# Performance work log

Measured on AMD Instinct MI355X. Metric: run time of the kernel, lower is better.

Reference implementation:

```python
import jax, jax.numpy as jnp
import numpy as np

TIME_STEP = 0.02  # matches init_kwargs
B, T, D = 128, 2048, 4


def setup_inputs() -> dict:
    key = jax.random.key(0)
    k1, k2, k3, k4 = jax.random.split(key, 4)
    return {
        "h_real": jax.random.normal(k1, (B, T, D, D), dtype=jnp.float32),
        "h_imag": jax.random.normal(k2, (B, T, D, D), dtype=jnp.float32),
        "s_real": jax.random.normal(k3, (B, D, D), dtype=jnp.float32),
        "s_imag": jax.random.normal(k4, (B, D, D), dtype=jnp.float32),
    }


def reference(h_real, h_imag, s_real, s_imag):
    # dt = -1j * time_step (complex64 scalar, as in the keras cell)
    dt = jnp.asarray(-1j * TIME_STEP, dtype=jnp.complex64)
    H = (h_real + 1j * h_imag).astype(jnp.complex64)        # [B,T,D,D]
    state0 = (s_real + 1j * s_imag).astype(jnp.complex64)    # [B,D,D]
    Hs = jnp.transpose(H, (1, 0, 2, 3))                       # [T,B,D,D] for scan

    def step(state, h_t):
        # unitary = expm(-i*dt*H_t), batched over B via expm's leading-dim batching
        unitary = jax.scipy.linalg.expm(h_t * dt)             # [B,D,D]
        new_state = jnp.matmul(unitary, state)                # [B,D,D]
        return new_state, new_state

    _, seq = jax.lax.scan(step, state0, Hs)                   # seq: [T,B,D,D] complex64
    # return real/imag stacked so downstream harness sees a real tensor
    return jnp.stack([seq.real, seq.imag])                    # [2,T,B,D,D] float32
```

## Files before the change

kernel.cpp:

```cpp
#include <hip/hip_runtime.h>

namespace {

constexpr int    TT    = 2048;
constexpr int    BB    = 128;
constexpr int    CHUNK = 8;
constexpr int    TPB   = 1024;
constexpr int    TLOC  = TPB / 2;
constexpr int    BPB   = TT / TLOC;
constexpr int    NBLK  = (BB / 2) * BPB;
constexpr int    NCH   = TLOC / CHUNK;
constexpr float  DT    = 0.02f;
constexpr size_t HALF  = (size_t)TT * BB * 16;

typedef float f32x4 __attribute__((ext_vector_type(4)));

__device__ __forceinline__ void cmm(const float* __restrict__ ar, const float* __restrict__ ai,
                                    const float* __restrict__ br, const float* __restrict__ bi,
                                    float* __restrict__ cr, float* __restrict__ ci) {
#pragma unroll
    for (int i = 0; i < 4; ++i) {
#pragma unroll
        for (int j = 0; j < 4; ++j) {
            float sr = 0.f, si = 0.f;
#pragma unroll
            for (int k = 0; k < 4; ++k) {
                const float xr = ar[i * 4 + k], xi = ai[i * 4 + k];
                const float yr = br[k * 4 + j], yi = bi[k * 4 + j];
                sr = fmaf(xr, yr, sr);
                sr = fmaf(-xi, yi, sr);
                si = fmaf(xr, yi, si);
                si = fmaf(xi, yr, si);
            }
            cr[i * 4 + j] = sr;
            ci[i * 4 + j] = si;
        }
    }
}

__device__ __forceinline__ void cmm_acc(const float* __restrict__ ar, const float* __restrict__ ai,
                                        const float* __restrict__ br, const float* __restrict__ bi,
                                        float* __restrict__ cr, float* __restrict__ ci) {
#pragma unroll
    for (int i = 0; i < 4; ++i) {
#pragma unroll
        for (int j = 0; j < 4; ++j) {
            float sr = cr[i * 4 + j], si = ci[i * 4 + j];
#pragma unroll
            for (int k = 0; k < 4; ++k) {
                const float xr = ar[i * 4 + k], xi = ai[i * 4 + k];
                const float yr = br[k * 4 + j], yi = bi[k * 4 + j];
                sr = fmaf(xr, yr, sr);
                sr = fmaf(-xi, yi, sr);
                si = fmaf(xr, yi, si);
                si = fmaf(xi, yr, si);
            }
            cr[i * 4 + j] = sr;
            ci[i * 4 + j] = si;
        }
    }
}

__device__ __forceinline__ void loadA(const float* __restrict__ hr, const float* __restrict__ hi,
                                      size_t gi, float* __restrict__ a_r, float* __restrict__ a_i) {
    const f32x4* p4r = reinterpret_cast<const f32x4*>(hr) + gi * 4;
    const f32x4* p4i = reinterpret_cast<const f32x4*>(hi) + gi * 4;
#pragma unroll
    for (int v = 0; v < 4; ++v) {
        const f32x4 rr = __builtin_nontemporal_load(p4r + v);
        const f32x4 im = __builtin_nontemporal_load(p4i + v);
#pragma unroll
        for (int e = 0; e < 4; ++e) {
            a_r[v * 4 + e] = DT * im[e];
            a_i[v * 4 + e] = -DT * rr[e];
        }
    }
}

__device__ __forceinline__ void expmPS(const float* __restrict__ a_r, const float* __restrict__ a_i,
                                       float* __restrict__ er, float* __restrict__ ei) {
    float a2r[16], a2i[16];
    cmm(a_r, a_i, a_r, a_i, a2r, a2i);
    float t6r[16], t6i[16];
#pragma unroll
    for (int e = 0; e < 16; ++e) {
        const float d = (e % 5 == 0) ? 1.0f : 0.0f;
        t6r[e] = fmaf(a_r[e], 1.f / 6.f, d * 0.5f);
        t6r[e] = fmaf(a2r[e], 1.f / 24.f, t6r[e]);
        t6i[e] = a_i[e] * (1.f / 6.f);
        t6i[e] = fmaf(a2i[e], 1.f / 24.f, t6i[e]);
        er[e]  = a_r[e] + d;
        ei[e]  = a_i[e];
    }
    cmm_acc(a2r, a2i, t6r, t6i, er, ei);
}

__device__ __forceinline__ unsigned int cp_load(unsigned int* p) {
    return __hip_atomic_fetch_add(p, 0u, __ATOMIC_RELAXED, __HIP_MEMORY_SCOPE_AGENT);
}
__device__ __forceinline__ void cp_store(unsigned int* p, unsigned int v) {
    (void)__hip_atomic_exchange(p, v, __ATOMIC_RELAXED, __HIP_MEMORY_SCOPE_AGENT);
}

}

__global__ void k_init(unsigned int* flag) { flag[threadIdx.x] = 0u; }

__global__ __launch_bounds__(TPB, 4) void k_main(
        const float* __restrict__ hr, const float* __restrict__ hi,
        const float* __restrict__ sr, const float* __restrict__ si,
        float* __restrict__ out, float* __restrict__ prefix,
        unsigned int* __restrict__ flag) {
    __shared__ float lds[24576];
    float* tot  = lds;
    float* carr = lds + 4096;

    const int tid    = threadIdx.x;
    const int bid    = blockIdx.x;
    const int blockT = bid & (BPB - 1);
    const int pair   = bid >> 2;
    const int b0     = pair * 2;
    const int pb     = tid & 1;
    const int tloc   = tid >> 1;
    const int t      = blockT * TLOC + tloc;
    const int b      = b0 + pb;
    const int lane   = tid & 63;
    const int sub    = (lane >> 1) & (CHUNK - 1);
    const int c      = tloc >> 3;

    float er[16], ei[16];
    {
        float a_r[16], a_i[16];
        loadA(hr, hi, (size_t)b * TT + t, a_r, a_i);
        expmPS(a_r, a_i, er, ei);
    }

#pragma unroll
    for (int d = 1; d < CHUNK; d <<= 1) {
        int src = lane - 2 * d;
        if (src < 0) src = 0;
        float qr[16], qi[16];
#pragma unroll
        for (int e = 0; e < 16; ++e) {
            qr[e] = __shfl(er[e], src, 64);
            qi[e] = __shfl(ei[e], src, 64);
        }
        float nr[16], ni[16];
        cmm(er, ei, qr, qi, nr, ni);
        const bool pred = (sub >= d);
#pragma unroll
        for (int e = 0; e < 16; ++e) {
            er[e] = pred ? nr[e] : er[e];
            ei[e] = pred ? ni[e] : ei[e];
        }
    }

    if (sub == CHUNK - 1) {
#pragma unroll
        for (int e = 0; e < 16; ++e) {
            tot[((pb << 5) + e) * NCH + c]      = er[e];
            tot[((pb << 5) + 16 + e) * NCH + c] = ei[e];
        }
    }
    __syncthreads();

    if (tid < 128) {
        const int w  = tid >> 6;
        const int cc = tid & 63;
        float ipr[16], ipi[16];
#pragma unroll
        for (int e = 0; e < 16; ++e) {
            ipr[e] = tot[((w << 5) + e) * NCH + cc];
            ipi[e] = tot[((w << 5) + 16 + e) * NCH + cc];
        }
#pragma unroll
        for (int d = 1; d < NCH; d <<= 1) {
            int src = cc - d;
            if (src < 0) src = 0;
            float qr[16], qi[16];
#pragma unroll
            for (int e = 0; e < 16; ++e) {
                qr[e] = __shfl(ipr[e], src, 64);
                qi[e] = __shfl(ipi[e], src, 64);
            }
            float nr[16], ni[16];
            cmm(ipr, ipi, qr, qi, nr, ni);
            const bool pred = (cc >= d);
#pragma unroll
            for (int e = 0; e < 16; ++e) {
                ipr[e] = pred ? nr[e] : ipr[e];
                ipi[e] = pred ? ni[e] : ipi[e];
            }
        }
#pragma unroll
        for (int e = 0; e < 16; ++e) {
            tot[((w << 5) + e) * NCH + cc]      = ipr[e];
            tot[((w << 5) + 16 + e) * NCH + cc] = ipi[e];
        }
    }

    if (tid == 0 && blockT != 0) {
        while (cp_load(flag + (bid - 1)) == 0u) {
            __builtin_amdgcn_s_sleep(2);
        }
    }
    __syncthreads();

    if (tid < 64) {
        const int ppb = tid >> 5, e = tid & 31;
        float pv;
        if (blockT == 0) {
            pv = (e < 16) ? sr[(b0 + ppb) * 16 + e] : si[(b0 + ppb) * 16 + (e - 16)];
        } else {
            pv = __uint_as_float(cp_load(
                reinterpret_cast<unsigned int*>(prefix) + (size_t)(bid - 1) * 64 + tid));
        }
        carr[(size_t)tid * (NCH + 1)] = pv;
    }
    __syncthreads();

    if (tid < 128) {
        const int w  = tid >> 6;
        const int cc = tid & 63;
        float Ppr[16], Ppi[16];
#pragma unroll
        for (int e = 0; e < 16; ++e) {
            Ppr[e] = carr[((w << 5) + e) * (NCH + 1)];
            Ppi[e] = carr[((w << 5) + 16 + e) * (NCH + 1)];
        }
        float cxr[16], cxi[16];
#pragma unroll
        for (int i = 0; i < 4; ++i) {
            float axr[4], axi[4];
#pragma unroll
            for (int k = 0; k < 4; ++k) {
                axr[k] = tot[((w << 5) + i * 4 + k) * NCH + cc];
                axi[k] = tot[((w << 5) + 16 + i * 4 + k) * NCH + cc];
            }
#pragma unroll
            for (int j = 0; j < 4; ++j) {
                float s_r = 0.f, s_i = 0.f;
#pragma unroll
                for (int k = 0; k < 4; ++k) {
                    s_r = fmaf(axr[k], Ppr[k * 4 + j], s_r);
                    s_r = fmaf(-axi[k], Ppi[k * 4 + j], s_r);
                    s_i = fmaf(axr[k], Ppi[k * 4 + j], s_i);
                    s_i = fmaf(axi[k], Ppr[k * 4 + j], s_i);
                }
                cxr[i * 4 + j] = s_r;
                cxi[i * 4 + j] = s_i;
            }
        }
#pragma unroll
        for (int e = 0; e < 16; ++e) {
            carr[((w << 5) + e) * (NCH + 1) + cc + 1]      = cxr[e];
            carr[((w << 5) + 16 + e) * (NCH + 1) + cc + 1] = cxi[e];
        }
    }
    __syncthreads();

    if (blockT != BPB - 1 && tid < 64) {
        const float v = carr[(size_t)tid * (NCH + 1) + NCH];
        cp_store(reinterpret_cast<unsigned int*>(prefix) + (size_t)bid * 64 + tid,
                 __float_as_uint(v));
        asm volatile("s_waitcnt vmcnt(0)" ::: "memory");
        if (tid == 0) cp_store(flag + bid, 1u);
    }

    {
        float c_r[16], c_i[16];
#pragma unroll
        for (int e = 0; e < 16; ++e) {
            c_r[e] = carr[((pb << 5) + e) * (NCH + 1) + c];
            c_i[e] = carr[((pb << 5) + 16 + e) * (NCH + 1) + c];
        }
        float o_r[16], o_i[16];
        cmm(er, ei, c_r, c_i, o_r, o_i);

        const size_t oi = ((size_t)t * BB + b) * 16;
        f32x4* orp = reinterpret_cast<f32x4*>(out + oi);
        f32x4* oip = reinterpret_cast<f32x4*>(out + HALF + oi);
#pragma unroll
        for (int w = 0; w < 4; ++w) {
            f32x4 vr, vi;
#pragma unroll
            for (int e = 0; e < 4; ++e) {
                vr[e] = o_r[w * 4 + e];
                vi[e] = o_i[w * 4 + e];
            }
            orp[w] = vr;
            oip[w] = vi;
        }
    }
}

extern "C" void kernel_launch(void* const* d_in, const int* in_sizes, int n_in,
                              void* d_out, int out_size, void* d_ws, size_t ws_size,
                              hipStream_t stream) {
    const float* hr = (const float*)d_in[0];
    const float* hi = (const float*)d_in[1];
    const float* sr = (const float*)d_in[2];
    const float* si = (const float*)d_in[3];
    float* out    = (float*)d_out;
    float* prefix = (float*)d_ws;
    unsigned int* flag = (unsigned int*)((float*)d_ws + (size_t)NBLK * 64);

    k_init<<<1, NBLK, 0, stream>>>(flag);
    k_main<<<NBLK, TPB, 0, stream>>>(hr, hi, sr, si, out, prefix, flag);
}
```

Before: 125.0 us.

## Decouple block prefix chain by publishing local totals and combining predecessors locally

Each block now publishes its local block-total product right away, without first waiting on its predecessor. After waiting for all earlier blocks' flags, it folds their totals with the initial state itself, so the serial decoupled-lookback chain across time blocks goes away. The per-chunk product with the in-block exclusive prefix is computed before the wait to overlap latency. The cost is redundant small matrix products per block, extra barriers in the combine loop, and a smaller shared-memory footprint that may raise occupancy.

```diff
diff --git a/kernel.cpp b/kernel.cpp
--- a/kernel.cpp
+++ b/kernel.cpp
@@ -111,9 +111,9 @@
         const float* __restrict__ sr, const float* __restrict__ si,
         float* __restrict__ out, float* __restrict__ prefix,
         unsigned int* __restrict__ flag) {
-    __shared__ float lds[24576];
-    float* tot  = lds;
-    float* carr = lds + 4096;
+    __shared__ float tot[2 * 32 * NCH];
+    __shared__ float Tbuf[3 * 64];
+    __shared__ float Pl[2 * 32];
 
     const int tid    = threadIdx.x;
     const int bid    = blockIdx.x;
@@ -198,84 +198,89 @@
             tot[((w << 5) + 16 + e) * NCH + cc] = ipi[e];
         }
     }
-
-    if (tid == 0 && blockT != 0) {
-        while (cp_load(flag + (bid - 1)) == 0u) {
-            __builtin_amdgcn_s_sleep(2);
-        }
-    }
     __syncthreads();
 
-    if (tid < 64) {
+    if (blockT != BPB - 1 && tid < 64) {
         const int ppb = tid >> 5, e = tid & 31;
-        float pv;
-        if (blockT == 0) {
-            pv = (e < 16) ? sr[(b0 + ppb) * 16 + e] : si[(b0 + ppb) * 16 + (e - 16)];
-        } else {
-            pv = __uint_as_float(cp_load(
-                reinterpret_cast<unsigned int*>(prefix) + (size_t)(bid - 1) * 64 + tid));
-        }
-        carr[(size_t)tid * (NCH + 1)] = pv;
-    }
-    __syncthreads();
-
-    if (tid < 128) {
-        const int w  = tid >> 6;
-        const int cc = tid & 63;
-        float Ppr[16], Ppi[16];
-#pragma unroll
-        for (int e = 0; e < 16; ++e) {
-            Ppr[e] = carr[((w << 5) + e) * (NCH + 1)];
-            Ppi[e] = carr[((w << 5) + 16 + e) * (NCH + 1)];
-        }
-        float cxr[16], cxi[16];
-#pragma unroll
-        for (int i = 0; i < 4; ++i) {
-            float axr[4], axi[4];
-#pragma unroll
-            for (int k = 0; k < 4; ++k) {
-                axr[k] = tot[((w << 5) + i * 4 + k) * NCH + cc];
-                axi[k] = tot[((w << 5) + 16 + i * 4 + k) * NCH + cc];
-            }
-#pragma unroll
-            for (int j = 0; j < 4; ++j) {
-                float s_r = 0.f, s_i = 0.f;
-#pragma unroll
-                for (int k = 0; k < 4; ++k) {
-                    s_r = fmaf(axr[k], Ppr[k * 4 + j], s_r);
-                    s_r = fmaf(-axi[k], Ppi[k * 4 + j], s_r);
-                    s_i = fmaf(axr[k], Ppi[k * 4 + j], s_i);
-                    s_i = fmaf(axi[k], Ppr[k * 4 + j], s_i);
-                }
-                cxr[i * 4 + j] = s_r;
-                cxi[i * 4 + j] = s_i;
-            }
-        }
-#pragma unroll
-        for (int e = 0; e < 16; ++e) {
-            carr[((w << 5) + e) * (NCH + 1) + cc + 1]      = cxr[e];
-            carr[((w << 5) + 16 + e) * (NCH + 1) + cc + 1] = cxi[e];
-        }
-    }
-    __syncthreads();
-
-    if (blockT != BPB - 1 && tid < 64) {
-        const float v = carr[(size_t)tid * (NCH + 1) + NCH];
+        const float v = tot[((ppb << 5) + e) * NCH + (NCH - 1)];
         cp_store(reinterpret_cast<unsigned int*>(prefix) + (size_t)bid * 64 + tid,
                  __float_as_uint(v));
         asm volatile("s_waitcnt vmcnt(0)" ::: "memory");
         if (tid == 0) cp_store(flag + bid, 1u);
     }
 
+    float m_r[16], m_i[16];
+    if (c == 0) {
+#pragma unroll
+        for (int e = 0; e < 16; ++e) { m_r[e] = er[e]; m_i[e] = ei[e]; }
+    } else {
+        float ipr[16], ipi[16];
+#pragma unroll
+        for (int e = 0; e < 16; ++e) {
+            ipr[e] = tot[((pb << 5) + e) * NCH + (c - 1)];
+            ipi[e] = tot[((pb << 5) + 16 + e) * NCH + (c - 1)];
+        }
+        cmm(er, ei, ipr, ipi, m_r, m_i);
+    }
+
+    if (tid == 0 && blockT != 0) {
+        const int p0 = bid - blockT;
+        for (;;) {
+            unsigned int got = 0;
+            for (int k = 0; k < blockT; ++k) got += cp_load(flag + p0 + k);
+            if (got >= (unsigned int)blockT) break;
+            __builtin_amdgcn_s_sleep(2);
+        }
+    }
+    __syncthreads();
+
+    if (tid < 64 * blockT) {
+        const int p0 = bid - blockT;
+        const int k = tid >> 6, idx = tid & 63;
+        Tbuf[tid] = __uint_as_float(cp_load(
+            reinterpret_cast<unsigned int*>(prefix) + (size_t)(p0 + k) * 64 + idx));
+    }
+    if (tid < 64) {
+        const int ppb = tid >> 5, e = tid & 31;
+        Pl[tid] = (e < 16) ? sr[(b0 + ppb) * 16 + e] : si[(b0 + ppb) * 16 + (e - 16)];
+    }
+    __syncthreads();
+
+    for (int k = 0; k < blockT; ++k) {
+        const int w = tid >> 6, l = tid & 63;
+        const bool act = (tid < 128) && (l < 16);
+        float nr = 0.f, ni = 0.f;
+        if (act) {
+            const int i = l >> 2, j = l & 3;
+#pragma unroll
+            for (int kk = 0; kk < 4; ++kk) {
+                const float tr = Tbuf[k * 64 + (w << 5) + i * 4 + kk];
+                const float ti = Tbuf[k * 64 + (w << 5) + 16 + i * 4 + kk];
+                const float pr = Pl[(w << 5) + kk * 4 + j];
+                const float pi = Pl[(w << 5) + 16 + kk * 4 + j];
+                nr = fmaf(tr, pr, nr);
+                nr = fmaf(-ti, pi, nr);
+                ni = fmaf(tr, pi, ni);
+                ni = fmaf(ti, pr, ni);
+            }
+        }
+        __syncthreads();
+        if (act) {
+            Pl[(w << 5) + l]      = nr;
+            Pl[(w << 5) + 16 + l] = ni;
+        }
+        __syncthreads();
+    }
+
     {
-        float c_r[16], c_i[16];
-#pragma unroll
-        for (int e = 0; e < 16; ++e) {
-            c_r[e] = carr[((pb << 5) + e) * (NCH + 1) + c];
-            c_i[e] = carr[((pb << 5) + 16 + e) * (NCH + 1) + c];
+        float p_r[16], p_i[16];
+#pragma unroll
+        for (int e = 0; e < 16; ++e) {
+            p_r[e] = Pl[(pb << 5) + e];
+            p_i[e] = Pl[(pb << 5) + 16 + e];
         }
         float o_r[16], o_i[16];
-        cmm(er, ei, c_r, c_i, o_r, o_i);
+        cmm(m_r, m_i, p_r, p_i, o_r, o_i);
 
         const size_t oi = ((size_t)t * BB + b) * 16;
         f32x4* orp = reinterpret_cast<f32x4*>(out + oi);
```

New measurement: 115.6 us. 7.6% less time.
